# Performance work log

Hardware: AMD Instinct MI355X
Metric: run time of the kernel (lower is better)

The kernel has to match this reference:

```python
import jax, jax.numpy as jnp
import numpy as np

B, S, F = 4, 2048, 512
H, DK, DV, FILT = 8, 64, 64, 512

def setup_inputs() -> dict:
    key = jax.random.key(0)
    ks = jax.random.split(key, 11)
    sc_in = 1.0 / np.sqrt(F)
    sc_o = 1.0 / np.sqrt(H * DV)
    return {
        "x_q": jax.random.normal(ks[0], (B, S, F), jnp.float32),
        "x_k": jax.random.normal(ks[1], (B, S, F), jnp.float32),
        "x_v": jax.random.normal(ks[2], (B, S, F), jnp.float32),
        "Wq": jax.random.normal(ks[3], (H, F, DK), jnp.float32) * sc_in,
        "bq": jax.random.normal(ks[4], (H, DK), jnp.float32) * 0.01,
        "Wk": jax.random.normal(ks[5], (H, F, DK), jnp.float32) * sc_in,
        "bk": jax.random.normal(ks[6], (H, DK), jnp.float32) * 0.01,
        "Wv": jax.random.normal(ks[7], (H, F, DV), jnp.float32) * sc_in,
        "bv": jax.random.normal(ks[8], (H, DV), jnp.float32) * 0.01,
        "Wo": jax.random.normal(ks[9], (H * DV, FILT), jnp.float32) * sc_o,
        "bo": jax.random.normal(ks[10], (FILT,), jnp.float32) * 0.01,
    }

def reference(x_q, x_k, x_v, Wq, bq, Wk, bk, Wv, bv, Wo, bo):
    d_k = Wq.shape[-1]
    # per-head Dense projections, batched over heads: [B,H,S,dk/dv]
    q = jnp.einsum("bsf,hfk->bhsk", x_q, Wq) + bq[:, None, :]
    k = jnp.einsum("bsf,hfk->bhsk", x_k, Wk) + bk[:, None, :]
    v = jnp.einsum("bsf,hfv->bhsv", x_v, Wv) + bv[:, None, :]
    # scaled dot-product attention (scale by 1/sqrt(d_k) as in map_fn)
    scores = jnp.einsum("bhsk,bhtk->bhst", q, k) / jnp.sqrt(jnp.asarray(d_k, q.dtype))
    attn = jax.nn.softmax(scores, axis=-1)
    out = jnp.einsum("bhst,bhtv->bhsv", attn, v)
    # concat heads along feature dim -> [B,S,H*DV], then output linear
    bsz, h, s, dv = out.shape
    concat = out.transpose(0, 2, 1, 3).reshape(bsz, s, h * dv)
    return concat @ Wo + bo
```

## Files before the change

### kernel.cpp

```cpp
#include <hip/hip_runtime.h>

#define B_    4
#define S_    2048
#define H_    8
#define M_    (B_ * S_)

typedef __bf16    bf16_t;
typedef _Float16  f16_t;
typedef __bf16   bf16x8 __attribute__((ext_vector_type(8)));
typedef __bf16   bf16x4 __attribute__((ext_vector_type(4)));
typedef _Float16 f16x8  __attribute__((ext_vector_type(8)));
typedef float    f32x16 __attribute__((ext_vector_type(16)));

union B8 { uint4 u; bf16x8 v; bf16_t e[8]; };
union B4 { uint2 u; bf16x4 v; bf16_t e[4]; };
union H8 { uint4 u; f16x8  v; f16_t  e[8]; };
union H4 { uint2 u; f16_t  e[4]; };

#define QSCALE 0.1803368801111204f

typedef const __attribute__((address_space(1))) unsigned int ga_u32;
typedef __attribute__((address_space(3))) unsigned int       ls_u32;
__device__ __forceinline__ void g2l16(const void* g, void* l) {
    __builtin_amdgcn_global_load_lds((ga_u32*)g, (ls_u32*)l, 16, 0, 0);
}

__global__ __launch_bounds__(256) void cast_x(
    const float* __restrict__ xq, const float* __restrict__ xk,
    const float* __restrict__ xv,
    bf16_t* __restrict__ dq, bf16_t* __restrict__ dk, bf16_t* __restrict__ dv)
{
    const int z = blockIdx.y;
    const float* src = z == 0 ? xq : z == 1 ? xk : xv;
    bf16_t*      dst = z == 0 ? dq : z == 1 ? dk : dv;
    const size_t base = (size_t)blockIdx.x * 4096 + threadIdx.x * 4;
    #pragma unroll
    for (int k = 0; k < 4; ++k) {
        const size_t i = base + (size_t)k * 1024;
        float4 v = *(const float4*)(src + i);
        B4 o;
        o.e[0] = (bf16_t)v.x; o.e[1] = (bf16_t)v.y;
        o.e[2] = (bf16_t)v.z; o.e[3] = (bf16_t)v.w;
        *(uint2*)(dst + i) = o.u;
    }
}

__global__ __launch_bounds__(256) void convert_weights(
    const float* __restrict__ w0, const float* __restrict__ w1,
    const float* __restrict__ w2, const float* __restrict__ wo,
    bf16_t* __restrict__ t0, bf16_t* __restrict__ t1,
    bf16_t* __restrict__ t2, f16_t* __restrict__ wot)
{
    __shared__ float T[64][65];
    const int z   = blockIdx.z;
    const int k0  = blockIdx.x * 64;
    const int tid = threadIdx.x;
    const int row = tid & 63, q4 = tid >> 6;

    if (z < 3) {
        const float* W  = z == 0 ? w0 : z == 1 ? w1 : w2;
        bf16_t*      Wt = z == 0 ? t0 : z == 1 ? t1 : t2;
        const int h = blockIdx.y;
        const float* Wh = W + (size_t)h * 512 * 64;
        #pragma unroll
        for (int i = 0; i < 4; ++i) {
            int fq = q4 * 4 + i;
            float4 v = *(const float4*)(Wh + (size_t)(k0 + row) * 64 + fq * 4);
            T[row][fq * 4 + 0] = v.x; T[row][fq * 4 + 1] = v.y;
            T[row][fq * 4 + 2] = v.z; T[row][fq * 4 + 3] = v.w;
        }
        __syncthreads();
        bf16_t* Wth = Wt + (size_t)h * 64 * 512;
        #pragma unroll
        for (int i = 0; i < 4; ++i) {
            int kq = q4 * 4 + i;
            B4 o;
            #pragma unroll
            for (int j = 0; j < 4; ++j) o.e[j] = (bf16_t)T[kq * 4 + j][row];
            *(uint2*)(Wth + (size_t)row * 512 + k0 + kq * 4) = o.u;
        }
    } else {
        const int n0 = blockIdx.y * 64;
        #pragma unroll
        for (int i = 0; i < 4; ++i) {
            int fq = q4 * 4 + i;
            float4 v = *(const float4*)(wo + (size_t)(k0 + row) * 512 + n0 + fq * 4);
            T[row][fq * 4 + 0] = v.x; T[row][fq * 4 + 1] = v.y;
            T[row][fq * 4 + 2] = v.z; T[row][fq * 4 + 3] = v.w;
        }
        __syncthreads();
        #pragma unroll
        for (int i = 0; i < 4; ++i) {
            int kq = q4 * 4 + i;
            H4 o;
            #pragma unroll
            for (int j = 0; j < 4; ++j) o.e[j] = (f16_t)T[kq * 4 + j][row];
            *(uint2*)(wot + (size_t)(n0 + row) * 512 + k0 + kq * 4) = o.u;
        }
    }
}

__global__ __launch_bounds__(256) void proj_tiled(
    const bf16_t* __restrict__ xq, const bf16_t* __restrict__ xk,
    const bf16_t* __restrict__ xv,
    const bf16_t* __restrict__ Wtq, const bf16_t* __restrict__ Wtk,
    const bf16_t* __restrict__ Wtv,
    const float* __restrict__ bq, const float* __restrict__ bk,
    const float* __restrict__ bv,
    bf16_t* __restrict__ Qb, bf16_t* __restrict__ Kb, bf16_t* __restrict__ Vt)
{
    __shared__ char sm[34816];
    bf16_t* As = (bf16_t*)sm;
    bf16_t* Bs = As + 128 * 64;

    const int z = blockIdx.z;
    const bf16_t* X    = z == 0 ? xq  : z == 1 ? xk  : xv;
    const bf16_t* Wt   = z == 0 ? Wtq : z == 1 ? Wtk : Wtv;
    const float*  bias = z == 0 ? bq  : z == 1 ? bk  : bv;

    const int tid  = threadIdx.x;
    const int wave = tid >> 6, lane = tid & 63;
    const int l31  = lane & 31, half = lane >> 5;
    const int m0   = blockIdx.x * 128;
    const int n0   = blockIdx.y * 128;
    const int mw   = (wave & 1) * 64;
    const int nw   = (wave >> 1) * 64;

    const int srow = lane >> 3;
    const int scol = (lane & 7) * 16;

    f32x16 acc[2][2];
    #pragma unroll
    for (int mt = 0; mt < 2; ++mt)
        #pragma unroll
        for (int nt = 0; nt < 2; ++nt)
            #pragma unroll
            for (int i = 0; i < 16; ++i) acc[mt][nt][i] = 0.0f;

    for (int k0 = 0; k0 < 512; k0 += 64) {
        __syncthreads();
        #pragma unroll
        for (int i = 0; i < 4; ++i) {
            const int inst = wave * 4 + i;
            const int row  = inst * 8 + srow;
            g2l16((const char*)X  + ((size_t)(m0 + row) * 512 + k0) * 2 + scol,
                  sm + inst * 1024);
            g2l16((const char*)Wt + ((size_t)(n0 + row) * 512 + k0) * 2 + scol,
                  sm + 16384 + inst * 1024);
        }
        __syncthreads();

        #pragma unroll
        for (int kc = 0; kc < 4; ++kc) {
            B8 a0, a1, b0, b1;
            a0.u = *(const uint4*)&As[(mw + l31)      * 64 + kc * 16 + half * 8];
            a1.u = *(const uint4*)&As[(mw + 32 + l31) * 64 + kc * 16 + half * 8];
            b0.u = *(const uint4*)&Bs[(nw + l31)      * 64 + kc * 16 + half * 8];
            b1.u = *(const uint4*)&Bs[(nw + 32 + l31) * 64 + kc * 16 + half * 8];
            acc[0][0] = __builtin_amdgcn_mfma_f32_32x32x16_bf16(a0.v, b0.v, acc[0][0], 0, 0, 0);
            acc[0][1] = __builtin_amdgcn_mfma_f32_32x32x16_bf16(a0.v, b1.v, acc[0][1], 0, 0, 0);
            acc[1][0] = __builtin_amdgcn_mfma_f32_32x32x16_bf16(a1.v, b0.v, acc[1][0], 0, 0, 0);
            acc[1][1] = __builtin_amdgcn_mfma_f32_32x32x16_bf16(a1.v, b1.v, acc[1][1], 0, 0, 0);
        }
    }

    if (z <= 1) {
        const float sc_ = (z == 0) ? QSCALE : 1.0f;
        bf16_t* Out = (z == 0) ? Qb : Kb;
        #pragma unroll
        for (int mt = 0; mt < 2; ++mt)
            #pragma unroll
            for (int nt = 0; nt < 2; ++nt) {
                int n = n0 + nw + nt * 32 + l31;
                float bv_ = bias[n];
                #pragma unroll
                for (int r = 0; r < 16; ++r) {
                    int m = m0 + mw + mt * 32 + (r & 3) + 8 * (r >> 2) + 4 * half;
                    Out[(size_t)m * 512 + n] = (bf16_t)((acc[mt][nt][r] + bv_) * sc_);
                }
            }
    } else {
        const int b  = m0 >> 11;
        const int sb = m0 & 2047;
        __syncthreads();
        #pragma unroll
        for (int mt = 0; mt < 2; ++mt)
            #pragma unroll
            for (int nt = 0; nt < 2; ++nt) {
                const int nl  = nw + nt * 32 + l31;
                const float bv_ = bias[n0 + nl];
                #pragma unroll
                for (int r = 0; r < 16; r += 2) {
                    const int ml = mw + mt * 32 + (r & 3) + 8 * (r >> 2) + 4 * half;
                    union { unsigned u; bf16_t e[2]; } pk;
                    pk.e[0] = (bf16_t)(acc[mt][nt][r]     + bv_);
                    pk.e[1] = (bf16_t)(acc[mt][nt][r + 1] + bv_);
                    *(unsigned*)(sm + nl * 272 + ml * 2) = pk.u;
                }
            }
        __syncthreads();
        const int dl16 = tid >> 4;
        const int cc   = tid & 15;
        #pragma unroll
        for (int p = 0; p < 8; ++p) {
            const int d_l = p * 16 + dl16;
            const int ng  = n0 + d_l;
            const int h   = ng >> 6, dd = ng & 63;
            uint4 val = *(const uint4*)(sm + d_l * 272 + cc * 16);
            *(uint4*)(Vt + ((size_t)((b * 8 + h) * 64 + dd)) * 2048 + sb + cc * 8) = val;
        }
    }
}

__global__ __launch_bounds__(512, 2) void attn_mfma(
    const bf16_t* __restrict__ Q, const bf16_t* __restrict__ K,
    const bf16_t* __restrict__ Vt, f16_t* __restrict__ O)
{
    __shared__ char smraw[71680];
    bf16_t* KsBuf = (bf16_t*)smraw;
    bf16_t* VsBuf = KsBuf + 2 * 64 * 72;

    const int bh  = blockIdx.y;
    const int b   = bh >> 3, h = bh & 7;
    const int q0  = blockIdx.x * 256;
    const int tid = threadIdx.x;
    const int wave = tid >> 6, lane = tid & 63;
    const int l31 = lane & 31, half = lane >> 5;
    const int qsub = wave & 3, ksplit = wave >> 2;

    bf16x8 qfA[4], qfB[4];
    {
        const bf16_t* qp = Q + ((size_t)(b * S_ + q0 + qsub * 64 + l31)) * 512 + h * 64 + half * 8;
        #pragma unroll
        for (int ks = 0; ks < 4; ++ks) {
            B8 t;
            t.u = *(const uint4*)(qp + ks * 16);              qfA[ks] = t.v;
            t.u = *(const uint4*)(qp + 32 * 512 + ks * 16);   qfB[ks] = t.v;
        }
    }

    f32x16 oA0, oA1, oB0, oB1;
    #pragma unroll
    for (int i = 0; i < 16; ++i) { oA0[i] = 0.0f; oA1[i] = 0.0f; oB0[i] = 0.0f; oB1[i] = 0.0f; }
    float lA = 0.0f, lB = 0.0f;

    const bf16_t* Kbase = K + ((size_t)b * S_) * 512 + h * 64;
    const bf16_t* Vbase = Vt + ((size_t)bh * 64) * 2048;

    const int sbuf = tid >> 8;
    const int p    = tid & 255;
    const int kr = p >> 3, kc8 = p & 7;
    const int vd = p >> 2, vj = p & 3;
    const int kqmap[4] = {0, 2, 1, 3};
    const int vkq = kqmap[vj];
    bf16_t* KsS = KsBuf + sbuf * (64 * 72);
    bf16_t* VsS = VsBuf + sbuf * (64 * 72);
    const bf16_t* KsC = KsBuf + ksplit * (64 * 72);
    const bf16_t* VsC = VsBuf + ksplit * (64 * 72);

    uint4 kreg0, kreg1;
    uint2 vreg[4];
    {
        const int tb = sbuf * 1024;
        kreg0 = *(const uint4*)(Kbase + (size_t)(tb + kr) * 512 + kc8 * 8);
        kreg1 = *(const uint4*)(Kbase + (size_t)(tb + kr + 32) * 512 + kc8 * 8);
        #pragma unroll
        for (int g = 0; g < 4; ++g)
            vreg[g] = *(const uint2*)(Vbase + (size_t)vd * 2048 + tb + g * 16 + vkq * 4);
    }

    for (int t0 = 0; t0 < 1024; t0 += 64) {
        __syncthreads();
        *(uint4*)&KsS[kr * 72 + kc8 * 8]        = kreg0;
        *(uint4*)&KsS[(kr + 32) * 72 + kc8 * 8] = kreg1;
        #pragma unroll
        for (int g = 0; g < 4; ++g)
            *(uint2*)&VsS[vd * 72 + g * 16 + vj * 4] = vreg[g];
        __syncthreads();

        if (t0 + 64 < 1024) {
            const int tb = sbuf * 1024 + t0 + 64;
            kreg0 = *(const uint4*)(Kbase + (size_t)(tb + kr) * 512 + kc8 * 8);
            kreg1 = *(const uint4*)(Kbase + (size_t)(tb + kr + 32) * 512 + kc8 * 8);
            #pragma unroll
            for (int g = 0; g < 4; ++g)
                vreg[g] = *(const uint2*)(Vbase + (size_t)vd * 2048 + tb + g * 16 + vkq * 4);
        }

        f32x16 s00, s01, s10, s11;
        #pragma unroll
        for (int i = 0; i < 16; ++i) { s00[i] = 0.0f; s01[i] = 0.0f; s10[i] = 0.0f; s11[i] = 0.0f; }
        #pragma unroll
        for (int ks = 0; ks < 4; ++ks) {
            B8 kk0, kk1;
            kk0.u = *(const uint4*)(&KsC[l31 * 72 + ks * 16 + half * 8]);
            kk1.u = *(const uint4*)(&KsC[(32 + l31) * 72 + ks * 16 + half * 8]);
            s00 = __builtin_amdgcn_mfma_f32_32x32x16_bf16(kk0.v, qfA[ks], s00, 0, 0, 0);
            s01 = __builtin_amdgcn_mfma_f32_32x32x16_bf16(kk0.v, qfB[ks], s01, 0, 0, 0);
            s10 = __builtin_amdgcn_mfma_f32_32x32x16_bf16(kk1.v, qfA[ks], s10, 0, 0, 0);
            s11 = __builtin_amdgcn_mfma_f32_32x32x16_bf16(kk1.v, qfB[ks], s11, 0, 0, 0);
        }

        float lsA = 0.0f, lsB = 0.0f;
        #pragma unroll
        for (int r = 0; r < 16; ++r) {
            s00[r] = __builtin_amdgcn_exp2f(s00[r]); lsA += s00[r];
            s10[r] = __builtin_amdgcn_exp2f(s10[r]); lsA += s10[r];
            s01[r] = __builtin_amdgcn_exp2f(s01[r]); lsB += s01[r];
            s11[r] = __builtin_amdgcn_exp2f(s11[r]); lsB += s11[r];
        }
        lA += lsA; lB += lsB;

        B8 pfA[4], pfB[4];
        #pragma unroll
        for (int j = 0; j < 8; ++j) {
            pfA[0].e[j] = (bf16_t)s00[j];
            pfA[1].e[j] = (bf16_t)s00[8 + j];
            pfA[2].e[j] = (bf16_t)s10[j];
            pfA[3].e[j] = (bf16_t)s10[8 + j];
            pfB[0].e[j] = (bf16_t)s01[j];
            pfB[1].e[j] = (bf16_t)s01[8 + j];
            pfB[2].e[j] = (bf16_t)s11[j];
            pfB[3].e[j] = (bf16_t)s11[8 + j];
        }

        #pragma unroll
        for (int c = 0; c < 4; ++c) {
            B8 va, vb;
            va.u = *(const uint4*)(&VsC[l31 * 72 + c * 16 + half * 8]);
            vb.u = *(const uint4*)(&VsC[(32 + l31) * 72 + c * 16 + half * 8]);
            oA0 = __builtin_amdgcn_mfma_f32_32x32x16_bf16(va.v, pfA[c].v, oA0, 0, 0, 0);
            oA1 = __builtin_amdgcn_mfma_f32_32x32x16_bf16(vb.v, pfA[c].v, oA1, 0, 0, 0);
            oB0 = __builtin_amdgcn_mfma_f32_32x32x16_bf16(va.v, pfB[c].v, oB0, 0, 0, 0);
            oB1 = __builtin_amdgcn_mfma_f32_32x32x16_bf16(vb.v, pfB[c].v, oB1, 0, 0, 0);
        }
    }

    lA += __shfl_xor(lA, 32);
    lB += __shfl_xor(lB, 32);
    __syncthreads();
    float* co = (float*)smraw;
    float* cl = co + 4 * 64 * 68;
    if (ksplit == 1) {
        float* reg = co + qsub * (64 * 68);
        #pragma unroll
        for (int r = 0; r < 16; ++r) {
            reg[r * 68 + lane]        = oA0[r];
            reg[(16 + r) * 68 + lane] = oA1[r];
            reg[(32 + r) * 68 + lane] = oB0[r];
            reg[(48 + r) * 68 + lane] = oB1[r];
        }
        cl[qsub * 128 + lane]      = lA;
        cl[qsub * 128 + 64 + lane] = lB;
    }
    __syncthreads();
    if (ksplit == 0) {
        float* reg = co + qsub * (64 * 68);
        float invA = 1.0f / (lA + cl[qsub * 128 + lane]);
        float invB = 1.0f / (lB + cl[qsub * 128 + 64 + lane]);
        f16_t* ObA = O + ((size_t)(b * S_ + q0 + qsub * 64 + l31)) * 512 + h * 64;
        f16_t* ObB = ObA + (size_t)32 * 512;
        #pragma unroll
        for (int g = 0; g < 4; ++g) {
            H4 a, c, e, f;
            #pragma unroll
            for (int j = 0; j < 4; ++j) {
                int r = g * 4 + j;
                a.e[j] = (f16_t)((oA0[r] + reg[r * 68 + lane])        * invA);
                c.e[j] = (f16_t)((oA1[r] + reg[(16 + r) * 68 + lane]) * invA);
                e.e[j] = (f16_t)((oB0[r] + reg[(32 + r) * 68 + lane]) * invB);
                f.e[j] = (f16_t)((oB1[r] + reg[(48 + r) * 68 + lane]) * invB);
            }
            int d = 8 * g + 4 * half;
            *(uint2*)(ObA + d)      = a.u;
            *(uint2*)(ObA + 32 + d) = c.u;
            *(uint2*)(ObB + d)      = e.u;
            *(uint2*)(ObB + 32 + d) = f.u;
        }
    }
}

__global__ __launch_bounds__(256) void gemm_out_tiled(
    const f16_t* __restrict__ A, const f16_t* __restrict__ Wot,
    const float* __restrict__ bias, float* __restrict__ C)
{
    __shared__ f16_t As[64 * 72];
    __shared__ f16_t Bs[64 * 72];

    const int tid  = threadIdx.x;
    const int wave = tid >> 6, lane = tid & 63;
    const int l31  = lane & 31, half = lane >> 5;
    const int m0   = blockIdx.x * 64;
    const int n0   = blockIdx.y * 64;
    const int mw   = (wave & 1) * 32;
    const int nw   = (wave >> 1) * 32;

    const int sr  = tid >> 2;
    const int so  = (tid & 3) * 16;

    uint4 pA0, pA1, pB0, pB1;
    {
        const f16_t* ap = A   + (size_t)(m0 + sr) * 512 + so;
        const f16_t* bp = Wot + (size_t)(n0 + sr) * 512 + so;
        pA0 = *(const uint4*)(ap); pA1 = *(const uint4*)(ap + 8);
        pB0 = *(const uint4*)(bp); pB1 = *(const uint4*)(bp + 8);
    }

    f32x16 acc;
    #pragma unroll
    for (int i = 0; i < 16; ++i) acc[i] = 0.0f;

    for (int k0 = 0; k0 < 512; k0 += 64) {
        __syncthreads();
        *(uint4*)&As[sr * 72 + so]     = pA0;
        *(uint4*)&As[sr * 72 + so + 8] = pA1;
        *(uint4*)&Bs[sr * 72 + so]     = pB0;
        *(uint4*)&Bs[sr * 72 + so + 8] = pB1;
        __syncthreads();
        if (k0 + 64 < 512) {
            const f16_t* ap = A   + (size_t)(m0 + sr) * 512 + k0 + 64 + so;
            const f16_t* bp = Wot + (size_t)(n0 + sr) * 512 + k0 + 64 + so;
            pA0 = *(const uint4*)(ap); pA1 = *(const uint4*)(ap + 8);
            pB0 = *(const uint4*)(bp); pB1 = *(const uint4*)(bp + 8);
        }

        #pragma unroll
        for (int kc = 0; kc < 4; ++kc) {
            H8 a, b;
            a.u = *(const uint4*)&As[(mw + l31) * 72 + kc * 16 + half * 8];
            b.u = *(const uint4*)&Bs[(nw + l31) * 72 + kc * 16 + half * 8];
            acc = __builtin_amdgcn_mfma_f32_32x32x16_f16(a.v, b.v, acc, 0, 0, 0);
        }
    }

    const int n = n0 + nw + l31;
    const float bias0 = bias[n];
    #pragma unroll
    for (int r = 0; r < 16; ++r) {
        int m = m0 + mw + (r & 3) + 8 * (r >> 2) + 4 * half;
        C[(size_t)m * 512 + n] = acc[r] + bias0;
    }
}

extern "C" void kernel_launch(void* const* d_in, const int* in_sizes, int n_in,
                              void* d_out, int out_size, void* d_ws, size_t ws_size,
                              hipStream_t stream)
{
    const float* x_q = (const float*)d_in[0];
    const float* x_k = (const float*)d_in[1];
    const float* x_v = (const float*)d_in[2];
    const float* Wq  = (const float*)d_in[3];
    const float* bq  = (const float*)d_in[4];
    const float* Wk  = (const float*)d_in[5];
    const float* bk  = (const float*)d_in[6];
    const float* Wv  = (const float*)d_in[7];
    const float* bv  = (const float*)d_in[8];
    const float* Wo  = (const float*)d_in[9];
    const float* bo  = (const float*)d_in[10];
    float* out = (float*)d_out;

    char* W = (char*)d_ws;
    bf16_t* Wtq = (bf16_t*)W;
    bf16_t* Wtk = Wtq + (size_t)8 * 64 * 512;
    bf16_t* Wtv = Wtk + (size_t)8 * 64 * 512;
    f16_t*  Wot = (f16_t*)(Wtv + (size_t)8 * 64 * 512);
    bf16_t* Qb  = (bf16_t*)(Wot + (size_t)512 * 512);
    bf16_t* Kb  = Qb + (size_t)M_ * 512;
    bf16_t* Vt  = Kb + (size_t)M_ * 512;
    f16_t*  AO  = (f16_t*)(Vt + (size_t)M_ * 512);

    bf16_t* Xqb = (bf16_t*)out;
    bf16_t* Xkb = Xqb + (size_t)M_ * 512;
    bf16_t* Xvb = (bf16_t*)AO;

    cast_x<<<dim3(1024, 3), 256, 0, stream>>>(x_q, x_k, x_v, Xqb, Xkb, Xvb);

    convert_weights<<<dim3(8, 8, 4), 256, 0, stream>>>(
        Wq, Wk, Wv, Wo, Wtq, Wtk, Wtv, Wot);

    proj_tiled<<<dim3(64, 4, 3), 256, 0, stream>>>(
        Xqb, Xkb, Xvb, Wtq, Wtk, Wtv, bq, bk, bv, Qb, Kb, Vt);

    attn_mfma<<<dim3(S_ / 256, B_ * H_), 512, 0, stream>>>(Qb, Kb, Vt, AO);

    gemm_out_tiled<<<dim3(128, 8), 256, 0, stream>>>(AO, Wot, bo, out);
}
```

Before: 195.0 us.

## Enlarge output GEMM tile to 128x128 with direct global-to-LDS loads

The output projection GEMM now uses 128x128 block tiles with each wave computing a 64x64 sub-tile via four 32x32 MFMA accumulators, and loads tiles straight into LDS using global_load_lds instead of register staging. This raises operand reuse per LDS read and cuts block count. In exchange, register prefetch overlap is dropped, LDS rows are unpadded (possible bank conflicts), and only 256 blocks are launched.

```diff
diff --git a/kernel.cpp b/kernel.cpp
--- a/kernel.cpp
+++ b/kernel.cpp
@@ -384,62 +384,68 @@
     const f16_t* __restrict__ A, const f16_t* __restrict__ Wot,
     const float* __restrict__ bias, float* __restrict__ C)
 {
-    __shared__ f16_t As[64 * 72];
-    __shared__ f16_t Bs[64 * 72];
+    __shared__ char sm[32768];
+    f16_t* As = (f16_t*)sm;
+    f16_t* Bs = As + 128 * 64;
 
     const int tid  = threadIdx.x;
     const int wave = tid >> 6, lane = tid & 63;
     const int l31  = lane & 31, half = lane >> 5;
-    const int m0   = blockIdx.x * 64;
-    const int n0   = blockIdx.y * 64;
-    const int mw   = (wave & 1) * 32;
-    const int nw   = (wave >> 1) * 32;
-
-    const int sr  = tid >> 2;
-    const int so  = (tid & 3) * 16;
-
-    uint4 pA0, pA1, pB0, pB1;
-    {
-        const f16_t* ap = A   + (size_t)(m0 + sr) * 512 + so;
-        const f16_t* bp = Wot + (size_t)(n0 + sr) * 512 + so;
-        pA0 = *(const uint4*)(ap); pA1 = *(const uint4*)(ap + 8);
-        pB0 = *(const uint4*)(bp); pB1 = *(const uint4*)(bp + 8);
-    }
-
-    f32x16 acc;
+    const int m0   = blockIdx.x * 128;
+    const int n0   = blockIdx.y * 128;
+    const int mw   = (wave & 1) * 64;
+    const int nw   = (wave >> 1) * 64;
+
+    const int srow = lane >> 3;
+    const int scol = (lane & 7) * 16;
+
+    f32x16 acc[2][2];
     #pragma unroll
-    for (int i = 0; i < 16; ++i) acc[i] = 0.0f;
+    for (int mt = 0; mt < 2; ++mt)
+        #pragma unroll
+        for (int nt = 0; nt < 2; ++nt)
+            #pragma unroll
+            for (int i = 0; i < 16; ++i) acc[mt][nt][i] = 0.0f;
 
     for (int k0 = 0; k0 < 512; k0 += 64) {
         __syncthreads();
-        *(uint4*)&As[sr * 72 + so]     = pA0;
-        *(uint4*)&As[sr * 72 + so + 8] = pA1;
-        *(uint4*)&Bs[sr * 72 + so]     = pB0;
-        *(uint4*)&Bs[sr * 72 + so + 8] = pB1;
-        __syncthreads();
-        if (k0 + 64 < 512) {
-            const f16_t* ap = A   + (size_t)(m0 + sr) * 512 + k0 + 64 + so;
-            const f16_t* bp = Wot + (size_t)(n0 + sr) * 512 + k0 + 64 + so;
-            pA0 = *(const uint4*)(ap); pA1 = *(const uint4*)(ap + 8);
-            pB0 = *(const uint4*)(bp); pB1 = *(const uint4*)(bp + 8);
-        }
+        #pragma unroll
+        for (int i = 0; i < 4; ++i) {
+            const int inst = wave * 4 + i;
+            const int row  = inst * 8 + srow;
+            g2l16((const char*)A   + ((size_t)(m0 + row) * 512 + k0) * 2 + scol,
+                  sm + inst * 1024);
+            g2l16((const char*)Wot + ((size_t)(n0 + row) * 512 + k0) * 2 + scol,
+                  sm + 16384 + inst * 1024);
+        }
+        __syncthreads();
 
         #pragma unroll
         for (int kc = 0; kc < 4; ++kc) {
-            H8 a, b;
-            a.u = *(const uint4*)&As[(mw + l31) * 72 + kc * 16 + half * 8];
-            b.u = *(const uint4*)&Bs[(nw + l31) * 72 + kc * 16 + half * 8];
-            acc = __builtin_amdgcn_mfma_f32_32x32x16_f16(a.v, b.v, acc, 0, 0, 0);
-        }
-    }
-
-    const int n = n0 + nw + l31;
-    const float bias0 = bias[n];
+            H8 a0, a1, b0, b1;
+            a0.u = *(const uint4*)&As[(mw + l31)      * 64 + kc * 16 + half * 8];
+            a1.u = *(const uint4*)&As[(mw + 32 + l31) * 64 + kc * 16 + half * 8];
+            b0.u = *(const uint4*)&Bs[(nw + l31)      * 64 + kc * 16 + half * 8];
+            b1.u = *(const uint4*)&Bs[(nw + 32 + l31) * 64 + kc * 16 + half * 8];
+            acc[0][0] = __builtin_amdgcn_mfma_f32_32x32x16_f16(a0.v, b0.v, acc[0][0], 0, 0, 0);
+            acc[0][1] = __builtin_amdgcn_mfma_f32_32x32x16_f16(a0.v, b1.v, acc[0][1], 0, 0, 0);
+            acc[1][0] = __builtin_amdgcn_mfma_f32_32x32x16_f16(a1.v, b0.v, acc[1][0], 0, 0, 0);
+            acc[1][1] = __builtin_amdgcn_mfma_f32_32x32x16_f16(a1.v, b1.v, acc[1][1], 0, 0, 0);
+        }
+    }
+
     #pragma unroll
-    for (int r = 0; r < 16; ++r) {
-        int m = m0 + mw + (r & 3) + 8 * (r >> 2) + 4 * half;
-        C[(size_t)m * 512 + n] = acc[r] + bias0;
-    }
+    for (int mt = 0; mt < 2; ++mt)
+        #pragma unroll
+        for (int nt = 0; nt < 2; ++nt) {
+            int n = n0 + nw + nt * 32 + l31;
+            float bias0 = bias[n];
+            #pragma unroll
+            for (int r = 0; r < 16; ++r) {
+                int m = m0 + mw + mt * 32 + (r & 3) + 8 * (r >> 2) + 4 * half;
+                C[(size_t)m * 512 + n] = acc[mt][nt][r] + bias0;
+            }
+        }
 }
 
 extern "C" void kernel_launch(void* const* d_in, const int* in_sizes, int n_in,
@@ -483,5 +489,5 @@
 
     attn_mfma<<<dim3(S_ / 256, B_ * H_), 512, 0, stream>>>(Qb, Kb, Vt, AO);
 
-    gemm_out_tiled<<<dim3(128, 8), 256, 0, stream>>>(AO, Wot, bo, out);
-}
+    gemm_out_tiled<<<dim3(64, 4), 256, 0, stream>>>(AO, Wot, bo, out);
+}
```

Result: slower. 200.6 us (+2.9%).
